# Kernel optimization log

Hardware: AMD Instinct MI355X
Metric: run time of the kernel (lower is better)

## Reference

```python
import jax, jax.numpy as jnp
import numpy as np

B1, B2 = 0.9, 0.999        # optax.adam defaults
LR, EPS = 0.1, 1e-8        # inner_gd_lr_y, adam eps (eps_root=0)
STEPS = 20                 # inner_gd_steps


def setup_inputs() -> dict:
    key = jax.random.key(0)
    ks = jax.random.split(key, 12)
    B, CD, W = 8192, 1, 32
    sc = 0.5
    return {
        "x": jax.random.normal(ks[0], (B, 1), dtype=jnp.float32),
        "c": jax.random.normal(ks[1], (B, CD), dtype=jnp.float32),
        "w0": sc * jax.random.normal(ks[2], (W, 2 + CD), dtype=jnp.float32),
        "b0": sc * jax.random.normal(ks[3], (W,), dtype=jnp.float32),
        "w1": sc * jax.random.normal(ks[4], (W, W), dtype=jnp.float32) / np.sqrt(W),
        "b1": sc * jax.random.normal(ks[5], (W,), dtype=jnp.float32),
        "w2": sc * jax.random.normal(ks[6], (W, W), dtype=jnp.float32) / np.sqrt(W),
        "b2": sc * jax.random.normal(ks[7], (W,), dtype=jnp.float32),
        "w3": sc * jax.random.normal(ks[8], (1, W), dtype=jnp.float32) / np.sqrt(W),
        "b3": sc * jax.random.normal(ks[9], (1,), dtype=jnp.float32),
        "y_mean": jnp.zeros((1,), dtype=jnp.float32),
    }


def reference(x, c, w0, b0, w1, b1, w2, b2, w3, b3, y_mean):
    def mlp(inp):  # inp: (3,) -> scalar energy
        h = jax.nn.relu(w0 @ inp + b0)
        h = jax.nn.relu(w1 @ h + b1)
        h = jax.nn.relu(w2 @ h + b2)
        return (w3 @ h + b3)[0]

    def base_energy(c_arg, x_i, y_arg):
        return mlp(jnp.concatenate([x_i, y_arg, c_arg]))

    # EBMUtils.get_c0_batch: nearest (non-self) neighbor in context space
    dists = jnp.linalg.norm(c[:, None, :] - c[None, :, :], axis=-1)
    dists = dists + jnp.eye(dists.shape[0], dtype=dists.dtype) * 1e9
    c0_batch = c[jnp.argmin(dists, axis=1)]

    def solve_one(x_i, c_fixed, c0):
        y0 = jnp.reshape(y_mean, (1,))
        c_init = jnp.zeros_like(c_fixed)
        state0 = (y0, c_init,
                  jnp.zeros_like(y0), jnp.zeros_like(y0),      # Adam m,v for y
                  jnp.zeros_like(c_init), jnp.zeros_like(c_init))  # Adam m,v for c

        def step(state, t):
            y, cc, my, vy, mc, vc = state

            def taylor_loss(y_arg):
                f = lambda c0a: base_energy(c0a, x_i, y_arg)
                E, dE = jax.jvp(f, (c0,), (cc - c0,))
                return E + dE

            gy = jax.grad(taylor_loss)(y)
            gc = jax.grad(lambda ca: base_energy(ca, x_i, y))(cc)

            def adam(g, m, v):
                m = B1 * m + (1.0 - B1) * g
                v = B2 * v + (1.0 - B2) * g * g
                mh = m / (1.0 - B1 ** t)
                vh = v / (1.0 - B2 ** t)
                return -LR * mh / (jnp.sqrt(vh) + EPS), m, v

            uy, my, vy = adam(gy, my, vy)
            uc, mc, vc = adam(gc, mc, vc)
            return (y + uy, cc + uc, my, vy, mc, vc), None

        (yf, cf, _, _, _, _), _ = jax.lax.scan(
            step, state0, jnp.arange(1, STEPS + 1, dtype=jnp.float32))
        return yf, cf

    pred, c_out = jax.vmap(solve_one)(x, c, c0_batch)
    return pred, c_out
```

## Files before the change

kernel.cpp:

```cpp
#include <hip/hip_runtime.h>

#define NB 8192
#define NSTEPS 20
#define DGATE 2e-3f

__global__ __launch_bounds__(256) void nn_kernel(const float* __restrict__ c,
                                                 int* __restrict__ nn) {
#pragma clang fp contract(off)
  __shared__ float cl[NB];
  const int tid = threadIdx.x;
  for (int k = tid; k < NB; k += 256) cl[k] = c[k];
  __syncthreads();
  const int wv = tid >> 6, lane = tid & 63;
  const int i = (blockIdx.x << 2) + wv;
  const float ci = cl[i];
  float bk = 1e30f;
  int bj = 0x7fffffff;
  for (int j = lane; j < NB; j += 64) {
    const float d = ci - cl[j];
    const float key = sqrtf(d * d);
    if (j != i && (key < bk || (key == bk && j < bj))) { bk = key; bj = j; }
  }
#pragma unroll
  for (int m = 1; m < 64; m <<= 1) {
    const float ok = __shfl_xor(bk, m);
    const int oj = __shfl_xor(bj, m);
    if (ok < bk || (ok == bk && oj < bj)) { bk = ok; bj = oj; }
  }
  if (lane == 0) nn[i] = bj;
}

#define DOT64_ROWLDS(dst, wp)                                   \
  { double a0_=0.,a1_=0.,a2_=0.,a3_=0.;                         \
    _Pragma("unroll")                                           \
    for (int q_=0;q_<8;++q_){                                   \
      const double2 hA_=hx2[2*q_], hB_=hx2[2*q_+1];             \
      a0_=fma((double)wp[i*33+4*q_+0],hA_.x,a0_);               \
      a1_=fma((double)wp[i*33+4*q_+1],hA_.y,a1_);               \
      a2_=fma((double)wp[i*33+4*q_+2],hB_.x,a2_);               \
      a3_=fma((double)wp[i*33+4*q_+3],hB_.y,a3_);}              \
    dst=(a0_+a1_)+(a2_+a3_); }

#define DOT64_LDS(dst, wp)                                      \
  { double a0_=0.,a1_=0.,a2_=0.,a3_=0.;                         \
    _Pragma("unroll")                                           \
    for (int q_=0;q_<8;++q_){                                   \
      const double2 hA_=hx2[2*q_], hB_=hx2[2*q_+1];             \
      a0_=fma((double)wp[(4*q_+0)*33+i],hA_.x,a0_);             \
      a1_=fma((double)wp[(4*q_+1)*33+i],hA_.y,a1_);             \
      a2_=fma((double)wp[(4*q_+2)*33+i],hB_.x,a2_);             \
      a3_=fma((double)wp[(4*q_+3)*33+i],hB_.y,a3_);}            \
    dst=(a0_+a1_)+(a2_+a3_); }

#define WROW1(j) w1p[i*33+(j)]
#define WROW2(j) w2p[i*33+(j)]
#define WCOL1(j) w1p[(j)*33+i]
#define WCOL2(j) w2p[(j)*33+i]
#define WGY(j) wgf[j]
#define F32DOT_ASC(acc, W)                                      \
  { acc=0.f; _Pragma("unroll")                                  \
    for (int j=0;j<32;++j) acc=fmaf(W(j), hxf[j], acc); }
#define F32DOT_DESC(acc, W)                                     \
  { acc=0.f; _Pragma("unroll")                                  \
    for (int j=31;j>=0;--j) acc=fmaf(W(j), hxf[j], acc); }

#define F32TRAJ(DOT)                                                   \
  {                                                                    \
    float y = ymf, cc = 0.f, my = 0.f, vy = 0.f, mc = 0.f, vc = 0.f;   \
    double p1d = 1.0, p2d = 1.0;                                       \
    for (int t = 0; t < NSTEPS; ++t) {                                 \
      p1d *= 0.9; p2d *= 0.999;                                        \
      const float bc1 = (float)(1.0 - p1d);                            \
      const float bc2 = (float)(1.0 - p2d);                            \
      const float cin = grp ? cc : c0f;                                \
      float a = 0.f;                                                   \
      a = fmaf(w0xf, xif, a); a = fmaf(w0yf, y, a);                    \
      a = fmaf(w0cf, cin, a);                                          \
      const float z0 = a + b0f; const float h0 = fmaxf(z0, 0.f);       \
      hxf[i] = h0; float sacc; DOT(sacc, WROW1);                       \
      const float z1 = sacc + b1f; const float h1 = fmaxf(z1, 0.f);    \
      hxf[i] = h1; DOT(sacc, WROW2);                                   \
      const float z2 = sacc + b2f;                                     \
      hxf[i] = z2 > 0.f ? w3f : 0.f; DOT(sacc, WCOL2);                 \
      const float g1 = z1 > 0.f ? sacc : 0.f;                          \
      hxf[i] = g1; DOT(sacc, WCOL1);                                   \
      const float g0 = z0 > 0.f ? sacc : 0.f;                          \
      hxf[i] = g0; DOT(sacc, WGY);                                     \
      const float gy = __shfl(sacc, 0);                                \
      const float gc = __shfl(sacc, 32);                               \
      { float tm = 0.9f * my, tg = 0.1f * gy; my = tm + tg;            \
        float tv = 0.999f * vy, t2 = 0.001f * gy; t2 = t2 * gy;        \
        vy = tv + t2;                                                  \
        const float mh = my / bc1, vh = vy / bc2;                      \
        const float den = sqrtf(vh) + 1e-8f;                           \
        y = y + (-0.1f * mh) / den; }                                  \
      { float tm = 0.9f * mc, tg = 0.1f * gc; mc = tm + tg;            \
        float tv = 0.999f * vc, t2 = 0.001f * gc; t2 = t2 * gc;        \
        vc = tv + t2;                                                  \
        const float mh = mc / bc1, vh = vc / bc2;                      \
        const float den = sqrtf(vh) + 1e-8f;                           \
        cc = cc + (-0.1f * mh) / den; }                                \
    }                                                                  \
    yf = (double)y; cf = (double)cc;                                   \
  }

#define F64TRAJ(TRACKM)                                                \
  {                                                                    \
    double y = (double)ymf, cc = 0., my = 0., vy = 0., mc = 0.,        \
           vc = 0.;                                                    \
    double p1 = 1., p2 = 1.;                                           \
    for (int t = 0; t < NSTEPS; ++t) {                                 \
      p1 *= 0.9; p2 *= 0.999;                                          \
      const double cin = grp ? cc : (double)c0f;                       \
      const double z0 = fma((double)w0xf, (double)xif,                 \
                        fma((double)w0yf, y,                           \
                        fma((double)w0cf, cin, (double)b0f)));         \
      const bool m0 = z0 > zb;                                         \
      TRACKM(z0);                                                      \
      hx[i] = m0 ? z0 : 0.;                                            \
      double d1; DOT64_ROWLDS(d1, w1p);                                \
      const double z1 = d1 + (double)b1f;                              \
      const bool m1 = z1 > zb;                                         \
      TRACKM(z1);                                                      \
      hx[i] = m1 ? z1 : 0.;                                            \
      double d2; DOT64_ROWLDS(d2, w2p);                                \
      const double z2 = d2 + (double)b2f;                              \
      const bool m2 = z2 > zb;                                         \
      TRACKM(z2);                                                      \
      hx[i] = m2 ? (double)w3f : 0.;                                   \
      double s1; DOT64_LDS(s1, w2p);                                   \
      hx[i] = m1 ? s1 : 0.;                                            \
      double s0; DOT64_LDS(s0, w1p);                                   \
      const double g0 = m0 ? s0 : 0.;                                  \
      double gp = (double)wselF * g0;                                  \
      _Pragma("unroll")                                                \
      for (int msk = 1; msk < 32; msk <<= 1) gp += __shfl_xor(gp, msk);\
      const double gy = __shfl(gp, 0) + gb;                            \
      const double gc = __shfl(gp, 32) + gb;                           \
      my = 0.9 * my + 0.1 * gy;                                        \
      vy = 0.999 * vy + 0.001 * gy * gy;                               \
      y += -0.1 * (my / (1. - p1)) / (sqrt(vy / (1. - p2)) + 1e-8);    \
      mc = 0.9 * mc + 0.1 * gc;                                        \
      vc = 0.999 * vc + 0.001 * gc * gc;                               \
      cc += -0.1 * (mc / (1. - p1)) / (sqrt(vc / (1. - p2)) + 1e-8);   \
    }                                                                  \
    yf = y; cf = cc;                                                   \
  }

#define TRK(z) { minz = fmin(minz, fabs(z)); }
#define NOTRK(z)

#define FOLD()                                                         \
  { const float yF = (float)yf, cF = (float)cf;                        \
    if (fabsf(yF - yA) <= 0.07f && fabsf(cF - cA) <= 0.07f) {          \
      ymin = fminf(ymin, yF); ymax = fmaxf(ymax, yF);                  \
      cmin = fminf(cmin, cF); cmax = fmaxf(cmax, cF);                  \
    } }

#define STAGE_LDS()                                                    \
  for (int idx = tid; idx < 1024; idx += 256) {                        \
    const int r = idx >> 5, cl = idx & 31;                             \
    w1p[r * 33 + cl] = w1[idx];                                        \
    w2p[r * 33 + cl] = w2[idx];                                        \
  }                                                                    \
  if (tid < 32) {                                                      \
    w0yc[0][tid] = w0[tid * 3 + 1];                                    \
    w0yc[1][tid] = w0[tid * 3 + 2];                                    \
  }                                                                    \
  __syncthreads();

#define CONSTS_F32()                                                   \
  const float w0xf = w0[i*3+0], w0yf = w0[i*3+1], w0cf = w0[i*3+2];    \
  const float b0f = b0[i], b1f = b1[i], b2f = b2[i], w3f = w3[i];      \
  const float xif = x[s], c0f = c[nn[s]], ymf = y_mean[0];             \
  const float wselF = grp ? w0cf : w0yf;

#define IDX()                                                          \
  const int tid = threadIdx.x;                                         \
  const int wv = tid >> 6;                                             \
  const int lane = tid & 63;                                           \
  const int grp = (lane >> 5) & 1;                                     \
  const int i = lane & 31;

__global__ __launch_bounds__(256) void ebm_p0_kernel(
    const float* __restrict__ x, const float* __restrict__ c,
    const float* __restrict__ w0, const float* __restrict__ b0,
    const float* __restrict__ w1, const float* __restrict__ b1,
    const float* __restrict__ w2, const float* __restrict__ b2,
    const float* __restrict__ w3, const float* __restrict__ y_mean,
    const int* __restrict__ nn, float* __restrict__ p0buf) {
  __shared__ double hbuf[4][2][32];
  __shared__ float w1p[32 * 33];
  __shared__ float w2p[32 * 33];
  __shared__ float w0yc[2][32];
  IDX();
  const int s = (blockIdx.x << 2) + wv;
  STAGE_LDS();
  CONSTS_F32();
  double* hx = &hbuf[wv][grp][0];
  const double2* hx2 = (const double2*)hx;

  double yf, cf;
  double minz = 1e300;
  {
    const double zb = 0.0, gb = 0.0;
    F64TRAJ(TRK);
  }
#pragma unroll
  for (int msk = 1; msk < 64; msk <<= 1)
    minz = fmin(minz, __shfl_xor(minz, msk));

  if (lane == 0) {
    p0buf[0 * NB + s] = (float)yf;
    p0buf[1 * NB + s] = (float)cf;
    p0buf[2 * NB + s] = (float)minz;
  }
}

__global__ __launch_bounds__(256) void ebm_f32_kernel(
    const float* __restrict__ x, const float* __restrict__ c,
    const float* __restrict__ w0, const float* __restrict__ b0,
    const float* __restrict__ w1, const float* __restrict__ b1,
    const float* __restrict__ w2, const float* __restrict__ b2,
    const float* __restrict__ w3, const float* __restrict__ y_mean,
    const int* __restrict__ nn, const float* __restrict__ p0buf,
    float* __restrict__ out, int* __restrict__ list,
    int* __restrict__ count, float* __restrict__ base) {
  __shared__ float hfbuf[4][2][32];
  __shared__ float w1p[32 * 33];
  __shared__ float w2p[32 * 33];
  __shared__ float w0yc[2][32];
  IDX();
  const int s = (blockIdx.x << 2) + wv;
  STAGE_LDS();
  CONSTS_F32();
  float* hxf = &hfbuf[wv][grp][0];
  const float* wgf = &w0yc[grp][0];

  const float yA = p0buf[0 * NB + s], cA = p0buf[1 * NB + s];
  const float mzf = p0buf[2 * NB + s];
  float ymin = yA, ymax = yA, cmin = cA, cmax = cA;

  double yf, cf;
  {
#pragma clang fp contract(off)
    F32TRAJ(F32DOT_ASC)
  }
  const float y5 = (float)yf, c5 = (float)cf;
  FOLD();
  {
#pragma clang fp contract(off)
    F32TRAJ(F32DOT_DESC)
  }
  const float y6 = (float)yf, c6 = (float)cf;
  FOLD();

  const bool flag = (mzf <= 1e-5f) ||
                    (fabsf(y5 - yA) > DGATE) || (fabsf(c5 - cA) > DGATE) ||
                    (fabsf(y6 - yA) > DGATE) || (fabsf(c6 - cA) > DGATE);

  if (lane == 0) {
    out[s] = 0.5f * (ymin + ymax);
    out[NB + s] = 0.5f * (cmin + cmax);
    if (flag) {
      const int k = atomicAdd(count, 1);
      list[k] = s;
      base[0 * NB + s] = yA;   base[1 * NB + s] = cA;
      base[2 * NB + s] = ymin; base[3 * NB + s] = ymax;
      base[4 * NB + s] = cmin; base[5 * NB + s] = cmax;
    }
  }
}

__global__ __launch_bounds__(256) void ebm_flag_kernel(
    const float* __restrict__ x, const float* __restrict__ c,
    const float* __restrict__ w0, const float* __restrict__ b0,
    const float* __restrict__ w1, const float* __restrict__ b1,
    const float* __restrict__ w2, const float* __restrict__ b2,
    const float* __restrict__ w3, const float* __restrict__ y_mean,
    const int* __restrict__ nn, float* __restrict__ out,
    const int* __restrict__ list, const int* __restrict__ count,
    const float* __restrict__ base) {
  const int nflag = *count;
  if ((blockIdx.x << 2) >= nflag) return;

  __shared__ double hbuf[4][2][32];
  __shared__ float w1p[32 * 33];
  __shared__ float w2p[32 * 33];
  __shared__ float w0yc[2][32];
  IDX();
  const int k = (blockIdx.x << 2) + wv;
  const int s = list[k < nflag ? k : 0];
  STAGE_LDS();
  CONSTS_F32();
  double* hx = &hbuf[wv][grp][0];
  const double2* hx2 = (const double2*)hx;

  const float yA = base[0 * NB + s], cA = base[1 * NB + s];
  float ymin = base[2 * NB + s], ymax = base[3 * NB + s];
  float cmin = base[4 * NB + s], cmax = base[5 * NB + s];

  double yf, cf;
  for (int q = 1; q <= 4; ++q) {
    const double zb = (q == 1) ? -1e-5 : (q == 2) ? 1e-5 : 0.0;
    const double gb = (q == 3) ? 1e-6 : (q == 4) ? -1e-6 : 0.0;
    F64TRAJ(NOTRK);
    FOLD();
  }

  if (lane == 0 && k < nflag) {
    out[s] = 0.5f * (ymin + ymax);
    out[NB + s] = 0.5f * (cmin + cmax);
  }
}

extern "C" void kernel_launch(void* const* d_in, const int* in_sizes, int n_in,
                              void* d_out, int out_size, void* d_ws, size_t ws_size,
                              hipStream_t stream) {
  const float* x = (const float*)d_in[0];
  const float* c = (const float*)d_in[1];
  const float* w0 = (const float*)d_in[2];
  const float* b0 = (const float*)d_in[3];
  const float* w1 = (const float*)d_in[4];
  const float* b1 = (const float*)d_in[5];
  const float* w2 = (const float*)d_in[6];
  const float* b2 = (const float*)d_in[7];
  const float* w3 = (const float*)d_in[8];
  const float* y_mean = (const float*)d_in[10];

  char* ws = (char*)d_ws;
  int* nn = (int*)ws;
  int* count = (int*)(ws + NB * 4);
  int* list = (int*)(ws + NB * 4 + 16);
  float* base = (float*)(ws + NB * 8 + 16);
  float* p0buf = (float*)(ws + NB * 8 + 16 + NB * 24);

  hipMemsetAsync(count, 0, 4, stream);
  nn_kernel<<<NB / 4, 256, 0, stream>>>(c, nn);
  ebm_p0_kernel<<<NB / 4, 256, 0, stream>>>(
      x, c, w0, b0, w1, b1, w2, b2, w3, y_mean, nn, p0buf);
  ebm_f32_kernel<<<NB / 4, 256, 0, stream>>>(
      x, c, w0, b0, w1, b1, w2, b2, w3, y_mean, nn, p0buf,
      (float*)d_out, list, count, base);
  ebm_flag_kernel<<<NB / 4, 256, 0, stream>>>(
      x, c, w0, b0, w1, b1, w2, b2, w3, y_mean, nn, (float*)d_out,
      list, count, base);
}
```

Measured before the change: 624.9 us.

## Run f64 and f32 trajectories concurrently and parallelise flagged perturbations across waves

The f64 reference trajectory and the two f32 trajectories now run in one launch, with alternating blocks taking each role, so they no longer wait on each other. A small gate kernel then folds the results and builds the flagged list. The flag kernel gives each flagged sample a whole block, with its four perturbed f64 trajectories on separate waves instead of a serial loop. This shortens the critical path of the flagged refinement but adds a kernel launch, and launches NB blocks that mostly exit early.

```diff
diff --git a/kernel.cpp b/kernel.cpp
--- a/kernel.cpp
+++ b/kernel.cpp
@@ -150,11 +150,10 @@
 #define TRK(z) { minz = fmin(minz, fabs(z)); }
 #define NOTRK(z)
 
-#define FOLD()                                                         \
-  { const float yF = (float)yf, cF = (float)cf;                        \
-    if (fabsf(yF - yA) <= 0.07f && fabsf(cF - cA) <= 0.07f) {          \
-      ymin = fminf(ymin, yF); ymax = fmaxf(ymax, yF);                  \
-      cmin = fminf(cmin, cF); cmax = fmaxf(cmax, cF);                  \
+#define FFOLD(yF, cF)                                                  \
+  { if (fabsf((yF) - yA) <= 0.07f && fabsf((cF) - cA) <= 0.07f) {      \
+      ymin = fminf(ymin, (yF)); ymax = fmaxf(ymax, (yF));              \
+      cmin = fminf(cmin, (cF)); cmax = fmaxf(cmax, (cF));              \
     } }
 
 #define STAGE_LDS()                                                    \
@@ -182,133 +181,129 @@
   const int grp = (lane >> 5) & 1;                                     \
   const int i = lane & 31;
 
-__global__ __launch_bounds__(256) void ebm_p0_kernel(
+__global__ __launch_bounds__(256) void ebm_fused_kernel(
     const float* __restrict__ x, const float* __restrict__ c,
     const float* __restrict__ w0, const float* __restrict__ b0,
     const float* __restrict__ w1, const float* __restrict__ b1,
     const float* __restrict__ w2, const float* __restrict__ b2,
     const float* __restrict__ w3, const float* __restrict__ y_mean,
-    const int* __restrict__ nn, float* __restrict__ p0buf) {
+    const int* __restrict__ nn, float* __restrict__ p0buf,
+    float* __restrict__ f32buf) {
   __shared__ double hbuf[4][2][32];
   __shared__ float w1p[32 * 33];
   __shared__ float w2p[32 * 33];
   __shared__ float w0yc[2][32];
   IDX();
-  const int s = (blockIdx.x << 2) + wv;
+  const int b = blockIdx.x;
+  const int role = b & 1;
+  const int s = ((b >> 1) << 2) + wv;
   STAGE_LDS();
   CONSTS_F32();
-  double* hx = &hbuf[wv][grp][0];
-  const double2* hx2 = (const double2*)hx;
-
-  double yf, cf;
-  double minz = 1e300;
-  {
-    const double zb = 0.0, gb = 0.0;
-    F64TRAJ(TRK);
-  }
+
+  if (role == 0) {
+    double* hx = &hbuf[wv][grp][0];
+    const double2* hx2 = (const double2*)hx;
+    double yf, cf;
+    double minz = 1e300;
+    {
+      const double zb = 0.0, gb = 0.0;
+      F64TRAJ(TRK);
+    }
 #pragma unroll
-  for (int msk = 1; msk < 64; msk <<= 1)
-    minz = fmin(minz, __shfl_xor(minz, msk));
-
-  if (lane == 0) {
-    p0buf[0 * NB + s] = (float)yf;
-    p0buf[1 * NB + s] = (float)cf;
-    p0buf[2 * NB + s] = (float)minz;
-  }
-}
-
-__global__ __launch_bounds__(256) void ebm_f32_kernel(
+    for (int msk = 1; msk < 64; msk <<= 1)
+      minz = fmin(minz, __shfl_xor(minz, msk));
+    if (lane == 0) {
+      p0buf[0 * NB + s] = (float)yf;
+      p0buf[1 * NB + s] = (float)cf;
+      p0buf[2 * NB + s] = (float)minz;
+    }
+  } else {
+    float* hxf = (float*)&hbuf[wv][grp][0];
+    const float* wgf = &w0yc[grp][0];
+    double yf, cf;
+    {
+#pragma clang fp contract(off)
+      F32TRAJ(F32DOT_ASC)
+    }
+    const float y5 = (float)yf, c5 = (float)cf;
+    {
+#pragma clang fp contract(off)
+      F32TRAJ(F32DOT_DESC)
+    }
+    if (lane == 0) {
+      f32buf[0 * NB + s] = y5;
+      f32buf[1 * NB + s] = c5;
+      f32buf[2 * NB + s] = (float)yf;
+      f32buf[3 * NB + s] = (float)cf;
+    }
+  }
+}
+
+__global__ __launch_bounds__(256) void gate_kernel(
+    const float* __restrict__ p0buf, const float* __restrict__ f32buf,
+    float* __restrict__ out, int* __restrict__ list,
+    int* __restrict__ count) {
+  const int s = blockIdx.x * 256 + threadIdx.x;
+  const float yA = p0buf[0 * NB + s], cA = p0buf[1 * NB + s];
+  const float mzf = p0buf[2 * NB + s];
+  const float y5 = f32buf[0 * NB + s], c5 = f32buf[1 * NB + s];
+  const float y6 = f32buf[2 * NB + s], c6 = f32buf[3 * NB + s];
+  float ymin = yA, ymax = yA, cmin = cA, cmax = cA;
+  FFOLD(y5, c5);
+  FFOLD(y6, c6);
+  out[s] = 0.5f * (ymin + ymax);
+  out[NB + s] = 0.5f * (cmin + cmax);
+  const bool flag = (mzf <= 1e-5f) ||
+                    (fabsf(y5 - yA) > DGATE) || (fabsf(c5 - cA) > DGATE) ||
+                    (fabsf(y6 - yA) > DGATE) || (fabsf(c6 - cA) > DGATE);
+  if (flag) {
+    const int k = atomicAdd(count, 1);
+    list[k] = s;
+  }
+}
+
+__global__ __launch_bounds__(256) void ebm_flag_kernel(
     const float* __restrict__ x, const float* __restrict__ c,
     const float* __restrict__ w0, const float* __restrict__ b0,
     const float* __restrict__ w1, const float* __restrict__ b1,
     const float* __restrict__ w2, const float* __restrict__ b2,
     const float* __restrict__ w3, const float* __restrict__ y_mean,
     const int* __restrict__ nn, const float* __restrict__ p0buf,
-    float* __restrict__ out, int* __restrict__ list,
-    int* __restrict__ count, float* __restrict__ base) {
-  __shared__ float hfbuf[4][2][32];
-  __shared__ float w1p[32 * 33];
-  __shared__ float w2p[32 * 33];
-  __shared__ float w0yc[2][32];
-  IDX();
-  const int s = (blockIdx.x << 2) + wv;
-  STAGE_LDS();
-  CONSTS_F32();
-  float* hxf = &hfbuf[wv][grp][0];
-  const float* wgf = &w0yc[grp][0];
-
-  const float yA = p0buf[0 * NB + s], cA = p0buf[1 * NB + s];
-  const float mzf = p0buf[2 * NB + s];
-  float ymin = yA, ymax = yA, cmin = cA, cmax = cA;
-
-  double yf, cf;
-  {
-#pragma clang fp contract(off)
-    F32TRAJ(F32DOT_ASC)
-  }
-  const float y5 = (float)yf, c5 = (float)cf;
-  FOLD();
-  {
-#pragma clang fp contract(off)
-    F32TRAJ(F32DOT_DESC)
-  }
-  const float y6 = (float)yf, c6 = (float)cf;
-  FOLD();
-
-  const bool flag = (mzf <= 1e-5f) ||
-                    (fabsf(y5 - yA) > DGATE) || (fabsf(c5 - cA) > DGATE) ||
-                    (fabsf(y6 - yA) > DGATE) || (fabsf(c6 - cA) > DGATE);
-
-  if (lane == 0) {
-    out[s] = 0.5f * (ymin + ymax);
-    out[NB + s] = 0.5f * (cmin + cmax);
-    if (flag) {
-      const int k = atomicAdd(count, 1);
-      list[k] = s;
-      base[0 * NB + s] = yA;   base[1 * NB + s] = cA;
-      base[2 * NB + s] = ymin; base[3 * NB + s] = ymax;
-      base[4 * NB + s] = cmin; base[5 * NB + s] = cmax;
-    }
-  }
-}
-
-__global__ __launch_bounds__(256) void ebm_flag_kernel(
-    const float* __restrict__ x, const float* __restrict__ c,
-    const float* __restrict__ w0, const float* __restrict__ b0,
-    const float* __restrict__ w1, const float* __restrict__ b1,
-    const float* __restrict__ w2, const float* __restrict__ b2,
-    const float* __restrict__ w3, const float* __restrict__ y_mean,
-    const int* __restrict__ nn, float* __restrict__ out,
-    const int* __restrict__ list, const int* __restrict__ count,
-    const float* __restrict__ base) {
+    const float* __restrict__ f32buf, float* __restrict__ out,
+    const int* __restrict__ list, const int* __restrict__ count) {
   const int nflag = *count;
-  if ((blockIdx.x << 2) >= nflag) return;
+  if (blockIdx.x >= nflag) return;
 
   __shared__ double hbuf[4][2][32];
   __shared__ float w1p[32 * 33];
   __shared__ float w2p[32 * 33];
   __shared__ float w0yc[2][32];
+  __shared__ float res[4][2];
   IDX();
-  const int k = (blockIdx.x << 2) + wv;
-  const int s = list[k < nflag ? k : 0];
+  const int s = list[blockIdx.x];
   STAGE_LDS();
   CONSTS_F32();
   double* hx = &hbuf[wv][grp][0];
   const double2* hx2 = (const double2*)hx;
 
-  const float yA = base[0 * NB + s], cA = base[1 * NB + s];
-  float ymin = base[2 * NB + s], ymax = base[3 * NB + s];
-  float cmin = base[4 * NB + s], cmax = base[5 * NB + s];
-
+  const int q = wv + 1;
+  const double zb = (q == 1) ? -1e-5 : (q == 2) ? 1e-5 : 0.0;
+  const double gb = (q == 3) ? 1e-6 : (q == 4) ? -1e-6 : 0.0;
   double yf, cf;
-  for (int q = 1; q <= 4; ++q) {
-    const double zb = (q == 1) ? -1e-5 : (q == 2) ? 1e-5 : 0.0;
-    const double gb = (q == 3) ? 1e-6 : (q == 4) ? -1e-6 : 0.0;
-    F64TRAJ(NOTRK);
-    FOLD();
-  }
-
-  if (lane == 0 && k < nflag) {
+  F64TRAJ(NOTRK);
+  if (lane == 0) {
+    res[wv][0] = (float)yf;
+    res[wv][1] = (float)cf;
+  }
+  __syncthreads();
+
+  if (tid == 0) {
+    const float yA = p0buf[0 * NB + s], cA = p0buf[1 * NB + s];
+    float ymin = yA, ymax = yA, cmin = cA, cmax = cA;
+    FFOLD(f32buf[0 * NB + s], f32buf[1 * NB + s]);
+    FFOLD(f32buf[2 * NB + s], f32buf[3 * NB + s]);
+#pragma unroll
+    for (int p = 0; p < 4; ++p) FFOLD(res[p][0], res[p][1]);
     out[s] = 0.5f * (ymin + ymax);
     out[NB + s] = 0.5f * (cmin + cmax);
   }
@@ -332,17 +327,16 @@
   int* nn = (int*)ws;
   int* count = (int*)(ws + NB * 4);
   int* list = (int*)(ws + NB * 4 + 16);
-  float* base = (float*)(ws + NB * 8 + 16);
-  float* p0buf = (float*)(ws + NB * 8 + 16 + NB * 24);
+  float* p0buf = (float*)(ws + NB * 8 + 16);
+  float* f32buf = (float*)(ws + NB * 8 + 16 + NB * 12);
 
   hipMemsetAsync(count, 0, 4, stream);
   nn_kernel<<<NB / 4, 256, 0, stream>>>(c, nn);
-  ebm_p0_kernel<<<NB / 4, 256, 0, stream>>>(
-      x, c, w0, b0, w1, b1, w2, b2, w3, y_mean, nn, p0buf);
-  ebm_f32_kernel<<<NB / 4, 256, 0, stream>>>(
-      x, c, w0, b0, w1, b1, w2, b2, w3, y_mean, nn, p0buf,
-      (float*)d_out, list, count, base);
-  ebm_flag_kernel<<<NB / 4, 256, 0, stream>>>(
-      x, c, w0, b0, w1, b1, w2, b2, w3, y_mean, nn, (float*)d_out,
-      list, count, base);
-}
+  ebm_fused_kernel<<<NB / 2, 256, 0, stream>>>(
+      x, c, w0, b0, w1, b1, w2, b2, w3, y_mean, nn, p0buf, f32buf);
+  gate_kernel<<<NB / 256, 256, 0, stream>>>(
+      p0buf, f32buf, (float*)d_out, list, count);
+  ebm_flag_kernel<<<NB, 256, 0, stream>>>(
+      x, c, w0, b0, w1, b1, w2, b2, w3, y_mean, nn, p0buf, f32buf,
+      (float*)d_out, list, count);
+}
```

New measurement: 587.5 us. -6.0%, faster.
